# Optimization experiments

Measured on AMD Instinct MI355X. Metric: run time of the kernel, lower is better.

Reference implementation:

```python
import jax, jax.numpy as jnp
import numpy as np

B, TAPS = 1048576, 32
SAMPLING_INTERVAL = 1.0


def setup_inputs() -> dict:
    key = jax.random.key(0)
    k1, k2 = jax.random.split(key)
    input_now = jax.random.normal(k1, (B, 1), dtype=jnp.float32)
    output_prev = jax.random.normal(k2, (B, TAPS), dtype=jnp.float32)
    # learned relax weight, init 0.5, constrained to [0.01, 0.95]
    relax = jnp.full((1,), 0.5, dtype=jnp.float32)
    return {"input_now": input_now, "output_prev": output_prev, "relax": relax}


def reference(input_now, output_prev, relax):
    # Discrete Laguerre filterbank tap recursion (single filterbank):
    #   out[0] = sqrt(r)*prev[0] + T*sqrt(1-r)*x
    #   out[i] = sqrt(r)*(prev[i] + out[i-1]) - prev[i-1]
    r = relax[0]
    sr = jnp.sqrt(r)
    s1mr = jnp.sqrt(1.0 - r)
    prev_t = output_prev.T  # [TAPS, B]
    out0 = sr * prev_t[0] + SAMPLING_INTERVAL * s1mr * input_now[:, 0]  # [B]

    def step(carry, inp):
        prev_i, prev_im1 = inp
        out_i = sr * (prev_i + carry) - prev_im1
        return out_i, out_i

    _, outs = jax.lax.scan(step, out0, (prev_t[1:], prev_t[:-1]))  # [TAPS-1, B]
    out = jnp.concatenate([out0[None, :], outs], axis=0).T  # [B, TAPS]
    return out
```

## Files before the change

kernel.cpp:

```cpp
#include <hip/hip_runtime.h>


#define TAPS 32

__global__ __launch_bounds__(256) void laguerre_kernel(
    const float* __restrict__ input_now,
    const float* __restrict__ output_prev,
    const float* __restrict__ relax,
    float* __restrict__ out,
    int nrows)
{
    int b = blockIdx.x * blockDim.x + threadIdx.x;
    if (b >= nrows) return;

    float r    = relax[0];
    float sr   = sqrtf(r);
    float s1mr = sqrtf(1.0f - r);

    float p[TAPS];
    const float4* pv = reinterpret_cast<const float4*>(output_prev + (size_t)b * TAPS);
    float4* pp = reinterpret_cast<float4*>(p);
#pragma unroll
    for (int j = 0; j < TAPS / 4; ++j) pp[j] = pv[j];

    float x = input_now[b];

    float o   = fmaf(sr, p[0], s1mr * x);
    float pm1 = p[0];
    p[0] = o;
#pragma unroll
    for (int i = 1; i < TAPS; ++i) {
        float pi = p[i];
        o = fmaf(sr, pi + o, -pm1);
        pm1 = pi;
        p[i] = o;
    }

    float4* ov = reinterpret_cast<float4*>(out + (size_t)b * TAPS);
#pragma unroll
    for (int j = 0; j < TAPS / 4; ++j) ov[j] = pp[j];
}

extern "C" void kernel_launch(void* const* d_in, const int* in_sizes, int n_in,
                              void* d_out, int out_size, void* d_ws, size_t ws_size,
                              hipStream_t stream) {
    const float* input_now   = (const float*)d_in[0];
    const float* output_prev = (const float*)d_in[1];
    const float* relax       = (const float*)d_in[2];
    float* out = (float*)d_out;

    int nrows = in_sizes[0];
    int block = 256;
    int grid  = (nrows + block - 1) / block;
    laguerre_kernel<<<grid, block, 0, stream>>>(input_now, output_prev, relax, out, nrows);
}
```

Measured before the change: 252.8 us.

## Stage rows through padded LDS for fully coalesced float4 global loads and stores

Instead of each thread loading its own 128-byte row with strided float4 accesses, the block cooperatively loads contiguous float4s into a padded shared-memory tile, and each thread then runs the recursion on its row from LDS. Results go back to LDS and are written out cooperatively as contiguous float4s. The aim is fully coalesced global traffic in place of per-thread strided access. In exchange it adds about 33KB of LDS per block, two barriers, and scalar LDS accesses with padding to avoid bank conflicts, which may limit occupancy.

```diff
diff --git a/kernel.cpp b/kernel.cpp
--- a/kernel.cpp
+++ b/kernel.cpp
@@ -1,7 +1,10 @@
 #include <hip/hip_runtime.h>
 
 
-#define TAPS 32
+#define TAPS   32
+#define QPR    (TAPS / 4)
+#define ROWSPB 256
+#define LROW   (TAPS + 1)
 
 __global__ __launch_bounds__(256) void laguerre_kernel(
     const float* __restrict__ input_now,
@@ -10,20 +13,38 @@
     float* __restrict__ out,
     int nrows)
 {
-    int b = blockIdx.x * blockDim.x + threadIdx.x;
-    if (b >= nrows) return;
+    __shared__ float lds[ROWSPB * LROW];
 
-    float r    = relax[0];
-    float sr   = sqrtf(r);
-    float s1mr = sqrtf(1.0f - r);
+    const int t = threadIdx.x;
+    const long long row0 = (long long)blockIdx.x * ROWSPB;
+    const int rowsHere  = min(ROWSPB, nrows - (int)row0);
+    const int quadsHere = rowsHere * QPR;
 
+    const float4* gin = reinterpret_cast<const float4*>(output_prev) + row0 * QPR;
+#pragma unroll
+    for (int k = 0; k < QPR; ++k) {
+        int g = t + k * ROWSPB;
+        if (g < quadsHere) {
+            float4 v = gin[g];
+            int r = g >> 3, q = g & 7;
+            float* dst = &lds[r * LROW + q * 4];
+            dst[0] = v.x; dst[1] = v.y; dst[2] = v.z; dst[3] = v.w;
+        }
+    }
+    __syncthreads();
+
+    float rr   = relax[0];
+    float sr   = sqrtf(rr);
+    float s1mr = sqrtf(1.0f - rr);
+
+    int  myRow  = (int)row0 + t;
+    bool active = myRow < nrows;
+    float x = active ? input_now[myRow] : 0.0f;
+
+    float* row = &lds[t * LROW];
     float p[TAPS];
-    const float4* pv = reinterpret_cast<const float4*>(output_prev + (size_t)b * TAPS);
-    float4* pp = reinterpret_cast<float4*>(p);
 #pragma unroll
-    for (int j = 0; j < TAPS / 4; ++j) pp[j] = pv[j];
-
-    float x = input_now[b];
+    for (int i = 0; i < TAPS; ++i) p[i] = row[i];
 
     float o   = fmaf(sr, p[0], s1mr * x);
     float pm1 = p[0];
@@ -35,10 +56,20 @@
         pm1 = pi;
         p[i] = o;
     }
+#pragma unroll
+    for (int i = 0; i < TAPS; ++i) row[i] = p[i];
+    __syncthreads();
 
-    float4* ov = reinterpret_cast<float4*>(out + (size_t)b * TAPS);
+    float4* gout = reinterpret_cast<float4*>(out) + row0 * QPR;
 #pragma unroll
-    for (int j = 0; j < TAPS / 4; ++j) ov[j] = pp[j];
+    for (int k = 0; k < QPR; ++k) {
+        int g = t + k * ROWSPB;
+        if (g < quadsHere) {
+            int r = g >> 3, q = g & 7;
+            const float* src = &lds[r * LROW + q * 4];
+            gout[g] = make_float4(src[0], src[1], src[2], src[3]);
+        }
+    }
 }
 
 extern "C" void kernel_launch(void* const* d_in, const int* in_sizes, int n_in,
@@ -50,7 +81,6 @@
     float* out = (float*)d_out;
 
     int nrows = in_sizes[0];
-    int block = 256;
-    int grid  = (nrows + block - 1) / block;
-    laguerre_kernel<<<grid, block, 0, stream>>>(input_now, output_prev, relax, out, nrows);
+    int grid  = (nrows + ROWSPB - 1) / ROWSPB;
+    laguerre_kernel<<<grid, ROWSPB, 0, stream>>>(input_now, output_prev, relax, out, nrows);
 }
```

New measurement: 239.2 us. 1.06x faster.

## Split each row's tap recursion across 8 lanes with a shuffle-based parallel scan

Applied to the files above, without the earlier changes.

Each row of 32 taps is now handled by 8 threads, each loading one float4, so global loads and stores are fully coalesced across the wavefront instead of each thread striding 128 bytes. The linear recurrence is reformulated as local first-order updates plus a Hillis-Steele scan over the 8 lanes using __shfl_up with powers of sr^4. This raises thread count eightfold and adds shuffle and extra-FMA overhead. The reassociation may change floating-point rounding slightly.

```diff
diff --git a/kernel.cpp b/kernel.cpp
--- a/kernel.cpp
+++ b/kernel.cpp
@@ -10,35 +10,53 @@
     float* __restrict__ out,
     int nrows)
 {
-    int b = blockIdx.x * blockDim.x + threadIdx.x;
-    if (b >= nrows) return;
+    const int tid = blockIdx.x * blockDim.x + threadIdx.x;
+    const int row = tid >> 3;
+    const int g   = tid & 7;
+    if (row >= nrows) return;
 
-    float r    = relax[0];
-    float sr   = sqrtf(r);
-    float s1mr = sqrtf(1.0f - r);
+    const float rr   = relax[0];
+    const float sr   = sqrtf(rr);
+    const float s1mr = sqrtf(1.0f - rr);
 
-    float p[TAPS];
-    const float4* pv = reinterpret_cast<const float4*>(output_prev + (size_t)b * TAPS);
-    float4* pp = reinterpret_cast<float4*>(p);
-#pragma unroll
-    for (int j = 0; j < TAPS / 4; ++j) pp[j] = pv[j];
+    const float4 pv = reinterpret_cast<const float4*>(output_prev)[tid];
+    const float  x  = input_now[row];
 
-    float x = input_now[b];
+    const float prevlast = __shfl_up(pv.w, 1, 8);
 
-    float o   = fmaf(sr, p[0], s1mr * x);
-    float pm1 = p[0];
-    p[0] = o;
-#pragma unroll
-    for (int i = 1; i < TAPS; ++i) {
-        float pi = p[i];
-        o = fmaf(sr, pi + o, -pm1);
-        pm1 = pi;
-        p[i] = o;
-    }
+    const float e0 = (g == 0) ? fmaf(sr, pv.x, s1mr * x)
+                              : fmaf(sr, pv.x, -prevlast);
+    const float e1 = fmaf(sr, pv.y, -pv.x);
+    const float e2 = fmaf(sr, pv.z, -pv.y);
+    const float e3 = fmaf(sr, pv.w, -pv.z);
 
-    float4* ov = reinterpret_cast<float4*>(out + (size_t)b * TAPS);
-#pragma unroll
-    for (int j = 0; j < TAPS / 4; ++j) ov[j] = pp[j];
+    const float w0 = e0;
+    const float w1 = fmaf(sr, w0, e1);
+    const float w2 = fmaf(sr, w1, e2);
+    const float w3 = fmaf(sr, w2, e3);
+
+    const float sr2 = sr * sr;
+    const float sr3 = sr2 * sr;
+    const float a   = sr2 * sr2;
+    const float a2  = a * a;
+    const float a4  = a2 * a2;
+
+    float t = w3;
+    float u;
+    u = __shfl_up(t, 1, 8); t = (g >= 1) ? fmaf(a,  u, t) : t;
+    u = __shfl_up(t, 2, 8); t = (g >= 2) ? fmaf(a2, u, t) : t;
+    u = __shfl_up(t, 4, 8); t = (g >= 4) ? fmaf(a4, u, t) : t;
+
+    float inc = __shfl_up(t, 1, 8);
+    inc = (g >= 1) ? inc : 0.0f;
+
+    float4 yv;
+    yv.x = fmaf(sr,  inc, w0);
+    yv.y = fmaf(sr2, inc, w1);
+    yv.z = fmaf(sr3, inc, w2);
+    yv.w = fmaf(a,   inc, w3);
+
+    reinterpret_cast<float4*>(out)[tid] = yv;
 }
 
 extern "C" void kernel_launch(void* const* d_in, const int* in_sizes, int n_in,
@@ -50,7 +68,8 @@
     float* out = (float*)d_out;
 
     int nrows = in_sizes[0];
+    long long threads = (long long)nrows * 8;
     int block = 256;
-    int grid  = (nrows + block - 1) / block;
-    laguerre_kernel<<<grid, block, 0, stream>>>(input_now, output_prev, relax, out, nrows);
+    long long grid = (threads + block - 1) / block;
+    laguerre_kernel<<<(int)grid, block, 0, stream>>>(input_now, output_prev, relax, out, nrows);
 }
```

Measured after the change: 226.4 us. 1.12x faster.
